# Kernel optimization log

Hardware: AMD Instinct MI355X
Metric: run time of the kernel (lower is better)

The kernel has to match this reference:

```python
import jax, jax.numpy as jnp
import numpy as np
from jax import lax

T, B, N_INP, N_HID, N_OUT = 512, 64, 64, 2048, 64


def setup_inputs() -> dict:
    key = jax.random.key(0)
    ks = jax.random.split(key, 8)
    scale = 0.9 / np.sqrt(N_HID)  # keep recurrence stable over T steps
    return {
        "x": jax.random.normal(ks[0], (T, B, N_INP), jnp.float32),
        "Wi_w": jax.random.normal(ks[1], (N_HID, N_INP), jnp.float32) / np.sqrt(N_INP),
        "Wi_b": jax.random.normal(ks[2], (N_HID,), jnp.float32) * 0.1,
        "Wh_w": jax.random.normal(ks[3], (N_HID, N_HID), jnp.float32) * scale,
        "A": jax.random.uniform(ks[4], (N_HID,), jnp.float32),
        "omega": jax.random.uniform(ks[5], (N_HID,), jnp.float32),
        "Wr_w": jax.random.normal(ks[6], (N_OUT, N_HID), jnp.float32) / np.sqrt(N_HID),
        "Wr_b": jax.random.normal(ks[7], (N_OUT,), jnp.float32) * 0.1,
    }


def reference(x, Wi_w, Wi_b, Wh_w, A, omega, Wr_w, Wr_b):
    # Precompute input projection for all timesteps: [T, B, n_hid]
    u = jnp.einsum("tbi,hi->tbh", x, Wi_w) + Wi_b
    state0 = jnp.ones((x.shape[1], Wh_w.shape[0]), x.dtype)

    def step(state, u_t):
        # state = A * cos(omega*state + Wi(x_t)) + Wh(state)
        new = A * jnp.cos(omega * state + u_t) + state @ Wh_w.T
        return new, None

    state, _ = lax.scan(step, state0, u)
    return state @ Wr_w.T + Wr_b  # readout on final state: [B, n_out]
```

## Files before the change

kernel.cpp:

```cpp
#include <hip/hip_runtime.h>


typedef _Float16 half_t;
typedef _Float16 half8 __attribute__((ext_vector_type(8)));
typedef float f32x4 __attribute__((ext_vector_type(4)));

#define NHID 2048
#define NOUT 64
#define ST_UNIT 65536
#define N_ROUNDS 256

#define MFMA16(A, B, C) __builtin_amdgcn_mfma_f32_16x16x32_f16(A, B, C, 0, 0, 0)


__device__ __forceinline__ half8 cvt8(float4 lo, float4 hi) {
  half8 h;
  h[0] = (half_t)lo.x; h[1] = (half_t)lo.y; h[2] = (half_t)lo.z; h[3] = (half_t)lo.w;
  h[4] = (half_t)hi.x; h[5] = (half_t)hi.y; h[6] = (half_t)hi.z; h[7] = (half_t)hi.w;
  return h;
}

__global__ void psrnn_init_kernel(unsigned* flags, uint4* st) {
  int g = blockIdx.x * blockDim.x + threadIdx.x;
  uint4 v; v.x = 0x3C003C00u; v.y = 0x3C003C00u; v.z = 0x3C003C00u; v.w = 0x3C003C00u;
  const int rep = g >> 12, local = g & 4095;
  st[rep * (ST_UNIT / 8) + local] = v;
  if (g < 1024) flags[g] = 0;
}

__global__ __launch_bounds__(256) void psrnn_transpose_kernel(
    const float* __restrict__ Wh, half_t* __restrict__ WT16) {
  __shared__ float tile[64][65];
  const int bi = blockIdx.x & 31, bj = blockIdx.x >> 5;
  const int rs = threadIdx.x >> 6, c = threadIdx.x & 63;
#pragma unroll
  for (int i = 0; i < 16; ++i) {
    const int row = rs * 16 + i;
    tile[row][c] = Wh[(size_t)(bi * 64 + row) * NHID + bj * 64 + c];
  }
  __syncthreads();
#pragma unroll
  for (int i = 0; i < 16; ++i) {
    const int row = rs * 16 + i;
    WT16[(size_t)(bj * 64 + row) * NHID + bi * 64 + c] = (half_t)tile[c][row];
  }
}

__global__ __launch_bounds__(256) void psrnn_w2_kernel(
    const float* __restrict__ Wh, const half_t* __restrict__ WT16,
    half_t* __restrict__ W2) {
  const int bi = blockIdx.x & 31, bj = blockIdx.x >> 5;
  const int w = threadIdx.x >> 6, lane = threadIdx.x & 63;
  const int lm = lane & 15, kg = lane >> 4;
  const int rowA = bi * 64 + w * 16 + lm;
  f32x4 acc[4];
#pragma unroll
  for (int bt = 0; bt < 4; ++bt) acc[bt] = (f32x4){0.f, 0.f, 0.f, 0.f};
  for (int c = 0; c < 64; ++c) {
    const float* pa = Wh + (size_t)rowA * NHID + c * 32 + kg * 8;
    half8 a = cvt8(*(const float4*)pa, *(const float4*)(pa + 4));
#pragma unroll
    for (int bt = 0; bt < 4; ++bt) {
      half8 b = *(const half8*)(WT16 + (size_t)(bj * 64 + bt * 16 + lm) * NHID + c * 32 + kg * 8);
      acc[bt] = MFMA16(a, b, acc[bt]);
    }
  }
#pragma unroll
  for (int bt = 0; bt < 4; ++bt)
#pragma unroll
    for (int r = 0; r < 4; ++r)
      W2[(size_t)(bi * 64 + w * 16 + kg * 4 + r) * NHID + bj * 64 + bt * 16 + lm] =
          (half_t)acc[bt][r];
}

__global__ __launch_bounds__(256, 1) void psrnn_main_kernel(
    const float* __restrict__ x,
    const float* __restrict__ Wi_w,
    const float* __restrict__ Wi_b,
    const float* __restrict__ Wh_w,
    const float* __restrict__ Av,
    const float* __restrict__ Om,
    const half_t* __restrict__ W2,
    unsigned* __restrict__ flags,
    half_t* __restrict__ St)
{
  __shared__ float ybuf[2][4][2][2][16][18];
  __shared__ float ubuf[2][2][2][16][18];

  const int tid = threadIdx.x, w = tid >> 6, lane = tid & 63;
  const int lm = lane & 15, kg = lane >> 4;
  const int rep = blockIdx.x & 3, slot = blockIdx.x >> 2;
  const int n0 = slot * 32, b0 = rep * 16;
  const int tpar = w >> 1, ntu = w & 1;

  half8 wb[2][16], w2b[2][16];
#pragma unroll
  for (int nt = 0; nt < 2; ++nt)
#pragma unroll
    for (int c = 0; c < 16; ++c) {
      const float* p = Wh_w + (size_t)(n0 + nt * 16 + lm) * NHID + (w * 512 + c * 32 + kg * 8);
      wb[nt][c] = cvt8(*(const float4*)p, *(const float4*)(p + 4));
      w2b[nt][c] = *(const half8*)(W2 + (size_t)(n0 + nt * 16 + lm) * NHID +
                                   (w * 512 + c * 32 + kg * 8));
    }
  half8 wi0, wi1;
  {
    const float* p = Wi_w + (size_t)(n0 + ntu * 16 + lm) * 64 + kg * 8;
    wi0 = cvt8(*(const float4*)p, *(const float4*)(p + 4));
    wi1 = cvt8(*(const float4*)(p + 32), *(const float4*)(p + 36));
  }

  const int m = tid >> 4, nn = tid & 15;
  float cA2[2], cOm2[2], cB2[2];
  int off2[2];
#pragma unroll
  for (int nt = 0; nt < 2; ++nt) {
    const int ng = n0 + nt * 16 + nn;
    cA2[nt] = Av[ng]; cOm2[nt] = Om[ng]; cB2[nt] = Wi_b[ng];
    off2[nt] = ((slot * 4 + nt * 2 + (nn >> 3)) * 16 + m) * 8 + (nn & 7);
  }
  float cpr[2];

  unsigned* const pollp = flags + rep * 256 + w * 64 + lane;
  unsigned* const myf   = flags + rep * 256 + slot * 4 + w;

  if (w < 2) {
    const float* xp = x + (size_t)(b0 + lm) * 64;
    float4 a0 = *(const float4*)(xp + kg * 8), a1 = *(const float4*)(xp + kg * 8 + 4);
    float4 a2 = *(const float4*)(xp + 32 + kg * 8), a3 = *(const float4*)(xp + 36 + kg * 8);
    f32x4 au = {0.f, 0.f, 0.f, 0.f};
    au = MFMA16(cvt8(a0, a1), wi0, au);
    au = MFMA16(cvt8(a2, a3), wi1, au);
#pragma unroll
    for (int r = 0; r < 4; ++r) ubuf[0][0][ntu][kg * 4 + r][lm] = au[r];
  }
  __syncthreads();
  {
    half_t* w0c = St + (size_t)rep * ST_UNIT + 32768;
#pragma unroll
    for (int nt = 0; nt < 2; ++nt) {
      const float u0 = ubuf[0][0][nt][m][nn] + cB2[nt];
      cpr[nt] = cA2[nt] * __cosf(cOm2[nt] * 1.0f + u0);
      unsigned hv = (unsigned)__builtin_bit_cast(unsigned short, (half_t)cpr[nt]);
      const half_t* sp = w0c + off2[nt];
      asm volatile("global_store_short %0, %1, off sc1" :: "v"(sp), "v"(hv) : "memory");
    }
    asm volatile("s_waitcnt vmcnt(0)" ::: "memory");
    if (lane == 0)
      __hip_atomic_store(myf, 1u, __ATOMIC_RELAXED, __HIP_MEMORY_SCOPE_AGENT);
  }
  float4 xr0, xr1, xr2, xr3;
  {
    const float* xp = x + ((size_t)(1 + tpar) * 64 + b0 + lm) * 64;
    xr0 = *(const float4*)(xp + kg * 8);  xr1 = *(const float4*)(xp + kg * 8 + 4);
    xr2 = *(const float4*)(xp + 32 + kg * 8); xr3 = *(const float4*)(xp + 36 + kg * 8);
  }

  int bR = 0;
  for (int k = 0; k < N_ROUNDS; ++k) {
    const int bW = (bR == 2) ? 0 : bR + 1;
    const half_t* rB = St + (size_t)(bR * 4 + rep) * ST_UNIT;
    half_t* wB       = St + (size_t)(bW * 4 + rep) * ST_UNIT;
    const int par = k & 1;

    {
      f32x4 au = {0.f, 0.f, 0.f, 0.f};
      au = MFMA16(cvt8(xr0, xr1), wi0, au);
      au = MFMA16(cvt8(xr2, xr3), wi1, au);
#pragma unroll
      for (int r = 0; r < 4; ++r) ubuf[par][tpar][ntu][kg * 4 + r][lm] = au[r];
    }

    {
      const unsigned tgt = (unsigned)(k + 1);
      unsigned v = __hip_atomic_load(pollp, __ATOMIC_RELAXED, __HIP_MEMORY_SCOPE_AGENT);
      while (!__all((int)(v >= tgt)))
        v = __hip_atomic_load(pollp, __ATOMIC_RELAXED, __HIP_MEMORY_SCOPE_AGENT);
    }

    const half_t* ps0 = rB + (w * 16) * 512 + kg * 128 + lm * 8;
    const half_t* ps1 = ps0 + 2048;
    const half_t* ps2 = ps0 + 4096;
    const half_t* ps3 = ps0 + 6144;
    const half_t* pc0 = ps0 + 32768;
    const half_t* pc1 = ps1 + 32768;
    const half_t* pc2 = ps2 + 32768;
    const half_t* pc3 = ps3 + 32768;
    float4 Sr[16], Cr[16];
    asm volatile(
        "global_load_dwordx4 %0, %32, off sc1\n\t"
        "global_load_dwordx4 %1, %32, off offset:1024 sc1\n\t"
        "global_load_dwordx4 %2, %32, off offset:2048 sc1\n\t"
        "global_load_dwordx4 %3, %32, off offset:3072 sc1\n\t"
        "global_load_dwordx4 %4, %33, off sc1\n\t"
        "global_load_dwordx4 %5, %33, off offset:1024 sc1\n\t"
        "global_load_dwordx4 %6, %33, off offset:2048 sc1\n\t"
        "global_load_dwordx4 %7, %33, off offset:3072 sc1\n\t"
        "global_load_dwordx4 %8, %34, off sc1\n\t"
        "global_load_dwordx4 %9, %34, off offset:1024 sc1\n\t"
        "global_load_dwordx4 %10, %34, off offset:2048 sc1\n\t"
        "global_load_dwordx4 %11, %34, off offset:3072 sc1\n\t"
        "global_load_dwordx4 %12, %35, off sc1\n\t"
        "global_load_dwordx4 %13, %35, off offset:1024 sc1\n\t"
        "global_load_dwordx4 %14, %35, off offset:2048 sc1\n\t"
        "global_load_dwordx4 %15, %35, off offset:3072 sc1\n\t"
        "global_load_dwordx4 %16, %36, off sc1\n\t"
        "global_load_dwordx4 %17, %36, off offset:1024 sc1\n\t"
        "global_load_dwordx4 %18, %36, off offset:2048 sc1\n\t"
        "global_load_dwordx4 %19, %36, off offset:3072 sc1\n\t"
        "global_load_dwordx4 %20, %37, off sc1\n\t"
        "global_load_dwordx4 %21, %37, off offset:1024 sc1\n\t"
        "global_load_dwordx4 %22, %37, off offset:2048 sc1\n\t"
        "global_load_dwordx4 %23, %37, off offset:3072 sc1\n\t"
        "global_load_dwordx4 %24, %38, off sc1\n\t"
        "global_load_dwordx4 %25, %38, off offset:1024 sc1\n\t"
        "global_load_dwordx4 %26, %38, off offset:2048 sc1\n\t"
        "global_load_dwordx4 %27, %38, off offset:3072 sc1\n\t"
        "global_load_dwordx4 %28, %39, off sc1\n\t"
        "global_load_dwordx4 %29, %39, off offset:1024 sc1\n\t"
        "global_load_dwordx4 %30, %39, off offset:2048 sc1\n\t"
        "global_load_dwordx4 %31, %39, off offset:3072 sc1\n\t"
        "s_waitcnt vmcnt(0)"
        : "=&v"(Sr[0]), "=&v"(Sr[1]), "=&v"(Sr[2]), "=&v"(Sr[3]),
          "=&v"(Sr[4]), "=&v"(Sr[5]), "=&v"(Sr[6]), "=&v"(Sr[7]),
          "=&v"(Sr[8]), "=&v"(Sr[9]), "=&v"(Sr[10]), "=&v"(Sr[11]),
          "=&v"(Sr[12]), "=&v"(Sr[13]), "=&v"(Sr[14]), "=&v"(Sr[15]),
          "=&v"(Cr[0]), "=&v"(Cr[1]), "=&v"(Cr[2]), "=&v"(Cr[3]),
          "=&v"(Cr[4]), "=&v"(Cr[5]), "=&v"(Cr[6]), "=&v"(Cr[7]),
          "=&v"(Cr[8]), "=&v"(Cr[9]), "=&v"(Cr[10]), "=&v"(Cr[11]),
          "=&v"(Cr[12]), "=&v"(Cr[13]), "=&v"(Cr[14]), "=&v"(Cr[15])
        : "v"(ps0), "v"(ps1), "v"(ps2), "v"(ps3),
          "v"(pc0), "v"(pc1), "v"(pc2), "v"(pc3)
        : "memory");

    f32x4 y1a0 = {0.f,0.f,0.f,0.f}, y1a1 = {0.f,0.f,0.f,0.f};
    f32x4 y23a0 = {0.f,0.f,0.f,0.f}, y23a1 = {0.f,0.f,0.f,0.f};
#pragma unroll
    for (int c = 0; c < 16; ++c) {
      half8 sf = __builtin_bit_cast(half8, Sr[c]);
      half8 cf = __builtin_bit_cast(half8, Cr[c]);
      y1a0 = MFMA16(sf, wb[0][c], y1a0);
      y1a1 = MFMA16(sf, wb[1][c], y1a1);
      y23a0 = MFMA16(cf, wb[0][c], y23a0);
      y23a1 = MFMA16(cf, wb[1][c], y23a1);
      y23a0 = MFMA16(sf, w2b[0][c], y23a0);
      y23a1 = MFMA16(sf, w2b[1][c], y23a1);
    }
#pragma unroll
    for (int r = 0; r < 4; ++r) {
      ybuf[par][w][0][0][kg * 4 + r][lm] = y1a0[r];
      ybuf[par][w][0][1][kg * 4 + r][lm] = y1a1[r];
      ybuf[par][w][1][0][kg * 4 + r][lm] = y23a0[r];
      ybuf[par][w][1][1][kg * 4 + r][lm] = y23a1[r];
    }
    __syncthreads();

#pragma unroll
    for (int nt = 0; nt < 2; ++nt) {
      const float y1v = ybuf[par][0][0][nt][m][nn] + ybuf[par][1][0][nt][m][nn] +
                        ybuf[par][2][0][nt][m][nn] + ybuf[par][3][0][nt][m][nn];
      const float y23v = ybuf[par][0][1][nt][m][nn] + ybuf[par][1][1][nt][m][nn] +
                         ybuf[par][2][1][nt][m][nn] + ybuf[par][3][1][nt][m][nn];
      const float u1 = ubuf[par][0][nt][m][nn] + cB2[nt];
      const float u2 = ubuf[par][1][nt][m][nn] + cB2[nt];
      const float s1 = cpr[nt] + y1v;
      const float c1 = cA2[nt] * __cosf(cOm2[nt] * s1 + u1);
      const float s2 = c1 + y23v;
      const float c2 = cA2[nt] * __cosf(cOm2[nt] * s2 + u2);
      cpr[nt] = c2;
      unsigned hs = (unsigned)__builtin_bit_cast(unsigned short, (half_t)s2);
      unsigned hc = (unsigned)__builtin_bit_cast(unsigned short, (half_t)c2);
      const half_t* sps = wB + off2[nt];
      const half_t* spc = wB + 32768 + off2[nt];
      asm volatile("global_store_short %0, %1, off sc1" :: "v"(sps), "v"(hs) : "memory");
      asm volatile("global_store_short %0, %1, off sc1" :: "v"(spc), "v"(hc) : "memory");
    }
    asm volatile("s_waitcnt vmcnt(0)" ::: "memory");
    if (lane == 0)
      __hip_atomic_store(myf, (unsigned)(k + 2), __ATOMIC_RELAXED, __HIP_MEMORY_SCOPE_AGENT);

    {
      int t = 2 * k + 3 + tpar;
      if (t > 511) t = 511;
      const float* xp = x + ((size_t)t * 64 + b0 + lm) * 64;
      xr0 = *(const float4*)(xp + kg * 8);  xr1 = *(const float4*)(xp + kg * 8 + 4);
      xr2 = *(const float4*)(xp + 32 + kg * 8); xr3 = *(const float4*)(xp + 36 + kg * 8);
    }
    bR = bW;
  }
}

__global__ __launch_bounds__(256) void psrnn_readout_kernel(
    const float* __restrict__ Wr_w,
    const float* __restrict__ Wr_b,
    const half_t* __restrict__ St,
    float* __restrict__ out)
{
  const int tid = threadIdx.x, v = tid >> 6, lane = tid & 63;
  const int lm = lane & 15, kg = lane >> 4;
  const int rep = blockIdx.x;
  const half_t* sb = St + (size_t)(1 * 4 + rep) * ST_UNIT;

  f32x4 acc = {0.f, 0.f, 0.f, 0.f};
  for (int cg = 0; cg < 64; ++cg) {
    half8 a = *(const half8*)(sb + (size_t)cg * 512 + kg * 128 + lm * 8);
    const float* p = Wr_w + (size_t)(v * 16 + lm) * NHID + cg * 32 + kg * 8;
    half8 b = cvt8(*(const float4*)p, *(const float4*)(p + 4));
    acc = MFMA16(a, b, acc);
  }
#pragma unroll
  for (int r = 0; r < 4; ++r) {
    const int bidx = rep * 16 + kg * 4 + r;
    out[bidx * NOUT + v * 16 + lm] = acc[r] + Wr_b[v * 16 + lm];
  }
}

extern "C" void kernel_launch(void* const* d_in, const int* in_sizes, int n_in,
                              void* d_out, int out_size, void* d_ws, size_t ws_size,
                              hipStream_t stream) {
  const float* x    = (const float*)d_in[0];
  const float* Wi_w = (const float*)d_in[1];
  const float* Wi_b = (const float*)d_in[2];
  const float* Wh_w = (const float*)d_in[3];
  const float* Av   = (const float*)d_in[4];
  const float* Om   = (const float*)d_in[5];
  const float* Wr_w = (const float*)d_in[6];
  const float* Wr_b = (const float*)d_in[7];

  unsigned* flags = (unsigned*)d_ws;
  half_t*   St    = (half_t*)((char*)d_ws + 4096);
  half_t*   W2    = (half_t*)((char*)d_ws + (2u << 20));
  half_t*   WT16  = (half_t*)((char*)d_ws + (2u << 20) + (8u << 20));

  psrnn_init_kernel<<<64, 256, 0, stream>>>(flags, (uint4*)St);
  psrnn_transpose_kernel<<<1024, 256, 0, stream>>>(Wh_w, WT16);
  psrnn_w2_kernel<<<1024, 256, 0, stream>>>(Wh_w, WT16, W2);
  psrnn_main_kernel<<<256, 256, 0, stream>>>(x, Wi_w, Wi_b, Wh_w, Av, Om, W2, flags, St);
  psrnn_readout_kernel<<<4, 256, 0, stream>>>(Wr_w, Wr_b, St, (float*)d_out);
}
```

Measured before the change: 1.280 ms.

## Map persistent blocks to XCDs and mirror state buffers for local-cache reads

The main recurrent kernel now reads the XCC id in hardware and assigns each block's batch replica and hidden slot from it through an atomic roster, so blocks of one replica share a die. The state is written twice: once with sc0 into a buffer read by local waves and once with sc1 into a buffer read by remote waves. This lets same-die readers hit a nearer cache level instead of going through the coherence point. The W2 precompute GEMM is also retiled to 128x128 blocks with an LDS-staged B operand, and dynamic LDS is requested to force one block per CU. The risks are that slot assignment depends on the hardware placing exactly 32 blocks on each XCD, and that the doubled stores add write traffic.

```diff
diff --git a/kernel.cpp b/kernel.cpp
--- a/kernel.cpp
+++ b/kernel.cpp
@@ -20,15 +20,18 @@
   return h;
 }
 
-__global__ void psrnn_init_kernel(unsigned* flags, uint4* st) {
+__global__ void psrnn_init_kernel(unsigned* flags, unsigned* roster,
+                                  uint4* stA, uint4* stB) {
   int g = blockIdx.x * blockDim.x + threadIdx.x;
   uint4 v; v.x = 0x3C003C00u; v.y = 0x3C003C00u; v.z = 0x3C003C00u; v.w = 0x3C003C00u;
   const int rep = g >> 12, local = g & 4095;
-  st[rep * (ST_UNIT / 8) + local] = v;
+  stA[rep * (ST_UNIT / 8) + local] = v;
+  stB[rep * (ST_UNIT / 8) + local] = v;
   if (g < 1024) flags[g] = 0;
-}
-
-__global__ __launch_bounds__(256) void psrnn_transpose_kernel(
+  else if (g < 1032) roster[g - 1024] = 0;
+}
+
+__global__ __launch_bounds__(256) void psrnn_conv_kernel(
     const float* __restrict__ Wh, half_t* __restrict__ WT16) {
   __shared__ float tile[64][65];
   const int bi = blockIdx.x & 31, bj = blockIdx.x >> 5;
@@ -49,28 +52,46 @@
 __global__ __launch_bounds__(256) void psrnn_w2_kernel(
     const float* __restrict__ Wh, const half_t* __restrict__ WT16,
     half_t* __restrict__ W2) {
-  const int bi = blockIdx.x & 31, bj = blockIdx.x >> 5;
-  const int w = threadIdx.x >> 6, lane = threadIdx.x & 63;
+  __shared__ half_t Bs[128][40];
+  const int bi = blockIdx.x & 15, bj = blockIdx.x >> 4;
+  const int tid = threadIdx.x, w = tid >> 6, lane = tid & 63;
   const int lm = lane & 15, kg = lane >> 4;
-  const int rowA = bi * 64 + w * 16 + lm;
-  f32x4 acc[4];
-#pragma unroll
-  for (int bt = 0; bt < 4; ++bt) acc[bt] = (f32x4){0.f, 0.f, 0.f, 0.f};
+  const int brow = tid >> 2, bseg = tid & 3;
+
+  f32x4 acc[2][8];
+#pragma unroll
+  for (int mt = 0; mt < 2; ++mt)
+#pragma unroll
+    for (int nt = 0; nt < 8; ++nt) acc[mt][nt] = (f32x4){0.f, 0.f, 0.f, 0.f};
+
   for (int c = 0; c < 64; ++c) {
-    const float* pa = Wh + (size_t)rowA * NHID + c * 32 + kg * 8;
-    half8 a = cvt8(*(const float4*)pa, *(const float4*)(pa + 4));
-#pragma unroll
-    for (int bt = 0; bt < 4; ++bt) {
-      half8 b = *(const half8*)(WT16 + (size_t)(bj * 64 + bt * 16 + lm) * NHID + c * 32 + kg * 8);
-      acc[bt] = MFMA16(a, b, acc[bt]);
-    }
-  }
-#pragma unroll
-  for (int bt = 0; bt < 4; ++bt)
-#pragma unroll
-    for (int r = 0; r < 4; ++r)
-      W2[(size_t)(bi * 64 + w * 16 + kg * 4 + r) * NHID + bj * 64 + bt * 16 + lm] =
-          (half_t)acc[bt][r];
+    __syncthreads();
+#pragma unroll
+    for (int i = 0; i < 2; ++i) {
+      const int row = brow + i * 64;
+      *(half8*)&Bs[row][bseg * 8] =
+          *(const half8*)(WT16 + (size_t)(bj * 128 + row) * NHID + c * 32 + bseg * 8);
+    }
+    __syncthreads();
+    const float* pa0 = Wh + (size_t)(bi * 128 + w * 32 + lm) * NHID + c * 32 + kg * 8;
+    const float* pa1 = pa0 + (size_t)16 * NHID;
+    half8 a0 = cvt8(*(const float4*)pa0, *(const float4*)(pa0 + 4));
+    half8 a1 = cvt8(*(const float4*)pa1, *(const float4*)(pa1 + 4));
+#pragma unroll
+    for (int nt = 0; nt < 8; ++nt) {
+      half8 b = *(const half8*)&Bs[nt * 16 + lm][kg * 8];
+      acc[0][nt] = MFMA16(a0, b, acc[0][nt]);
+      acc[1][nt] = MFMA16(a1, b, acc[1][nt]);
+    }
+  }
+#pragma unroll
+  for (int mt = 0; mt < 2; ++mt)
+#pragma unroll
+    for (int nt = 0; nt < 8; ++nt)
+#pragma unroll
+      for (int r = 0; r < 4; ++r)
+        W2[(size_t)(bi * 128 + w * 32 + mt * 16 + kg * 4 + r) * NHID +
+           bj * 128 + nt * 16 + lm] = (half_t)acc[mt][nt][r];
 }
 
 __global__ __launch_bounds__(256, 1) void psrnn_main_kernel(
@@ -82,15 +103,28 @@
     const float* __restrict__ Om,
     const half_t* __restrict__ W2,
     unsigned* __restrict__ flags,
-    half_t* __restrict__ St)
+    unsigned* __restrict__ roster,
+    half_t* __restrict__ StA,
+    half_t* __restrict__ StB)
 {
+  extern __shared__ char lds_force[];
   __shared__ float ybuf[2][4][2][2][16][18];
   __shared__ float ubuf[2][2][2][16][18];
+  __shared__ unsigned slot_sh;
+  (void)lds_force;
 
   const int tid = threadIdx.x, w = tid >> 6, lane = tid & 63;
   const int lm = lane & 15, kg = lane >> 4;
-  const int rep = blockIdx.x & 3, slot = blockIdx.x >> 2;
+
+  unsigned xcd;
+  asm volatile("s_getreg_b32 %0, hwreg(HW_REG_XCC_ID)" : "=s"(xcd));
+  const int rep    = (int)(xcd & 3u);
+  const int halfId = (int)((xcd >> 2) & 1u);
+  if (tid == 0) slot_sh = (unsigned)(halfId * 32) + (atomicAdd(&roster[xcd & 7u], 1u) & 31u);
+  __syncthreads();
+  const int slot = (int)slot_sh;
   const int n0 = slot * 32, b0 = rep * 16;
+  const bool locw = ((w >> 1) == halfId);
   const int tpar = w >> 1, ntu = w & 1;
 
   half8 wb[2][16], w2b[2][16];
@@ -136,14 +170,17 @@
   }
   __syncthreads();
   {
-    half_t* w0c = St + (size_t)rep * ST_UNIT + 32768;
+    half_t* cA_ = StA + (size_t)rep * ST_UNIT + 32768;
+    half_t* cB_ = StB + (size_t)rep * ST_UNIT + 32768;
 #pragma unroll
     for (int nt = 0; nt < 2; ++nt) {
       const float u0 = ubuf[0][0][nt][m][nn] + cB2[nt];
       cpr[nt] = cA2[nt] * __cosf(cOm2[nt] * 1.0f + u0);
       unsigned hv = (unsigned)__builtin_bit_cast(unsigned short, (half_t)cpr[nt]);
-      const half_t* sp = w0c + off2[nt];
-      asm volatile("global_store_short %0, %1, off sc1" :: "v"(sp), "v"(hv) : "memory");
+      const half_t* pA = cA_ + off2[nt];
+      const half_t* pB = cB_ + off2[nt];
+      asm volatile("global_store_short %0, %1, off sc0" :: "v"(pA), "v"(hv) : "memory");
+      asm volatile("global_store_short %0, %1, off sc1" :: "v"(pB), "v"(hv) : "memory");
     }
     asm volatile("s_waitcnt vmcnt(0)" ::: "memory");
     if (lane == 0)
@@ -159,8 +196,6 @@
   int bR = 0;
   for (int k = 0; k < N_ROUNDS; ++k) {
     const int bW = (bR == 2) ? 0 : bR + 1;
-    const half_t* rB = St + (size_t)(bR * 4 + rep) * ST_UNIT;
-    half_t* wB       = St + (size_t)(bW * 4 + rep) * ST_UNIT;
     const int par = k & 1;
 
     {
@@ -178,7 +213,8 @@
         v = __hip_atomic_load(pollp, __ATOMIC_RELAXED, __HIP_MEMORY_SCOPE_AGENT);
     }
 
-    const half_t* ps0 = rB + (w * 16) * 512 + kg * 128 + lm * 8;
+    const half_t* rb = (locw ? StA : StB) + (size_t)(bR * 4 + rep) * ST_UNIT;
+    const half_t* ps0 = rb + w * 8192 + kg * 128 + lm * 8;
     const half_t* ps1 = ps0 + 2048;
     const half_t* ps2 = ps0 + 4096;
     const half_t* ps3 = ps0 + 6144;
@@ -187,51 +223,54 @@
     const half_t* pc2 = ps2 + 32768;
     const half_t* pc3 = ps3 + 32768;
     float4 Sr[16], Cr[16];
-    asm volatile(
-        "global_load_dwordx4 %0, %32, off sc1\n\t"
-        "global_load_dwordx4 %1, %32, off offset:1024 sc1\n\t"
-        "global_load_dwordx4 %2, %32, off offset:2048 sc1\n\t"
-        "global_load_dwordx4 %3, %32, off offset:3072 sc1\n\t"
-        "global_load_dwordx4 %4, %33, off sc1\n\t"
-        "global_load_dwordx4 %5, %33, off offset:1024 sc1\n\t"
-        "global_load_dwordx4 %6, %33, off offset:2048 sc1\n\t"
-        "global_load_dwordx4 %7, %33, off offset:3072 sc1\n\t"
-        "global_load_dwordx4 %8, %34, off sc1\n\t"
-        "global_load_dwordx4 %9, %34, off offset:1024 sc1\n\t"
-        "global_load_dwordx4 %10, %34, off offset:2048 sc1\n\t"
-        "global_load_dwordx4 %11, %34, off offset:3072 sc1\n\t"
-        "global_load_dwordx4 %12, %35, off sc1\n\t"
-        "global_load_dwordx4 %13, %35, off offset:1024 sc1\n\t"
-        "global_load_dwordx4 %14, %35, off offset:2048 sc1\n\t"
-        "global_load_dwordx4 %15, %35, off offset:3072 sc1\n\t"
-        "global_load_dwordx4 %16, %36, off sc1\n\t"
-        "global_load_dwordx4 %17, %36, off offset:1024 sc1\n\t"
-        "global_load_dwordx4 %18, %36, off offset:2048 sc1\n\t"
-        "global_load_dwordx4 %19, %36, off offset:3072 sc1\n\t"
-        "global_load_dwordx4 %20, %37, off sc1\n\t"
-        "global_load_dwordx4 %21, %37, off offset:1024 sc1\n\t"
-        "global_load_dwordx4 %22, %37, off offset:2048 sc1\n\t"
-        "global_load_dwordx4 %23, %37, off offset:3072 sc1\n\t"
-        "global_load_dwordx4 %24, %38, off sc1\n\t"
-        "global_load_dwordx4 %25, %38, off offset:1024 sc1\n\t"
-        "global_load_dwordx4 %26, %38, off offset:2048 sc1\n\t"
-        "global_load_dwordx4 %27, %38, off offset:3072 sc1\n\t"
-        "global_load_dwordx4 %28, %39, off sc1\n\t"
-        "global_load_dwordx4 %29, %39, off offset:1024 sc1\n\t"
-        "global_load_dwordx4 %30, %39, off offset:2048 sc1\n\t"
-        "global_load_dwordx4 %31, %39, off offset:3072 sc1\n\t"
-        "s_waitcnt vmcnt(0)"
-        : "=&v"(Sr[0]), "=&v"(Sr[1]), "=&v"(Sr[2]), "=&v"(Sr[3]),
-          "=&v"(Sr[4]), "=&v"(Sr[5]), "=&v"(Sr[6]), "=&v"(Sr[7]),
-          "=&v"(Sr[8]), "=&v"(Sr[9]), "=&v"(Sr[10]), "=&v"(Sr[11]),
-          "=&v"(Sr[12]), "=&v"(Sr[13]), "=&v"(Sr[14]), "=&v"(Sr[15]),
-          "=&v"(Cr[0]), "=&v"(Cr[1]), "=&v"(Cr[2]), "=&v"(Cr[3]),
-          "=&v"(Cr[4]), "=&v"(Cr[5]), "=&v"(Cr[6]), "=&v"(Cr[7]),
-          "=&v"(Cr[8]), "=&v"(Cr[9]), "=&v"(Cr[10]), "=&v"(Cr[11]),
-          "=&v"(Cr[12]), "=&v"(Cr[13]), "=&v"(Cr[14]), "=&v"(Cr[15])
-        : "v"(ps0), "v"(ps1), "v"(ps2), "v"(ps3),
-          "v"(pc0), "v"(pc1), "v"(pc2), "v"(pc3)
-        : "memory");
+#define LOADS(SC)                                                         \
+    asm volatile(                                                         \
+        "global_load_dwordx4 %0, %32, off " SC "\n\t"                     \
+        "global_load_dwordx4 %1, %32, off offset:1024 " SC "\n\t"         \
+        "global_load_dwordx4 %2, %32, off offset:2048 " SC "\n\t"         \
+        "global_load_dwordx4 %3, %32, off offset:3072 " SC "\n\t"         \
+        "global_load_dwordx4 %4, %33, off " SC "\n\t"                     \
+        "global_load_dwordx4 %5, %33, off offset:1024 " SC "\n\t"         \
+        "global_load_dwordx4 %6, %33, off offset:2048 " SC "\n\t"         \
+        "global_load_dwordx4 %7, %33, off offset:3072 " SC "\n\t"         \
+        "global_load_dwordx4 %8, %34, off " SC "\n\t"                     \
+        "global_load_dwordx4 %9, %34, off offset:1024 " SC "\n\t"         \
+        "global_load_dwordx4 %10, %34, off offset:2048 " SC "\n\t"        \
+        "global_load_dwordx4 %11, %34, off offset:3072 " SC "\n\t"        \
+        "global_load_dwordx4 %12, %35, off " SC "\n\t"                    \
+        "global_load_dwordx4 %13, %35, off offset:1024 " SC "\n\t"        \
+        "global_load_dwordx4 %14, %35, off offset:2048 " SC "\n\t"        \
+        "global_load_dwordx4 %15, %35, off offset:3072 " SC "\n\t"        \
+        "global_load_dwordx4 %16, %36, off " SC "\n\t"                    \
+        "global_load_dwordx4 %17, %36, off offset:1024 " SC "\n\t"        \
+        "global_load_dwordx4 %18, %36, off offset:2048 " SC "\n\t"        \
+        "global_load_dwordx4 %19, %36, off offset:3072 " SC "\n\t"        \
+        "global_load_dwordx4 %20, %37, off " SC "\n\t"                    \
+        "global_load_dwordx4 %21, %37, off offset:1024 " SC "\n\t"        \
+        "global_load_dwordx4 %22, %37, off offset:2048 " SC "\n\t"        \
+        "global_load_dwordx4 %23, %37, off offset:3072 " SC "\n\t"        \
+        "global_load_dwordx4 %24, %38, off " SC "\n\t"                    \
+        "global_load_dwordx4 %25, %38, off offset:1024 " SC "\n\t"        \
+        "global_load_dwordx4 %26, %38, off offset:2048 " SC "\n\t"        \
+        "global_load_dwordx4 %27, %38, off offset:3072 " SC "\n\t"        \
+        "global_load_dwordx4 %28, %39, off " SC "\n\t"                    \
+        "global_load_dwordx4 %29, %39, off offset:1024 " SC "\n\t"        \
+        "global_load_dwordx4 %30, %39, off offset:2048 " SC "\n\t"        \
+        "global_load_dwordx4 %31, %39, off offset:3072 " SC "\n\t"        \
+        "s_waitcnt vmcnt(0)"                                              \
+        : "=&v"(Sr[0]), "=&v"(Sr[1]), "=&v"(Sr[2]), "=&v"(Sr[3]),         \
+          "=&v"(Sr[4]), "=&v"(Sr[5]), "=&v"(Sr[6]), "=&v"(Sr[7]),         \
+          "=&v"(Sr[8]), "=&v"(Sr[9]), "=&v"(Sr[10]), "=&v"(Sr[11]),       \
+          "=&v"(Sr[12]), "=&v"(Sr[13]), "=&v"(Sr[14]), "=&v"(Sr[15]),     \
+          "=&v"(Cr[0]), "=&v"(Cr[1]), "=&v"(Cr[2]), "=&v"(Cr[3]),         \
+          "=&v"(Cr[4]), "=&v"(Cr[5]), "=&v"(Cr[6]), "=&v"(Cr[7]),         \
+          "=&v"(Cr[8]), "=&v"(Cr[9]), "=&v"(Cr[10]), "=&v"(Cr[11]),       \
+          "=&v"(Cr[12]), "=&v"(Cr[13]), "=&v"(Cr[14]), "=&v"(Cr[15])      \
+        : "v"(ps0), "v"(ps1), "v"(ps2), "v"(ps3),                         \
+          "v"(pc0), "v"(pc1), "v"(pc2), "v"(pc3)                          \
+        : "memory")
+    if (locw) { LOADS("sc0"); } else { LOADS("sc1"); }
+#undef LOADS
 
     f32x4 y1a0 = {0.f,0.f,0.f,0.f}, y1a1 = {0.f,0.f,0.f,0.f};
     f32x4 y23a0 = {0.f,0.f,0.f,0.f}, y23a1 = {0.f,0.f,0.f,0.f};
@@ -255,6 +294,8 @@
     }
     __syncthreads();
 
+    half_t* wBA = StA + (size_t)(bW * 4 + rep) * ST_UNIT;
+    half_t* wBB = StB + (size_t)(bW * 4 + rep) * ST_UNIT;
 #pragma unroll
     for (int nt = 0; nt < 2; ++nt) {
       const float y1v = ybuf[par][0][0][nt][m][nn] + ybuf[par][1][0][nt][m][nn] +
@@ -270,10 +311,14 @@
       cpr[nt] = c2;
       unsigned hs = (unsigned)__builtin_bit_cast(unsigned short, (half_t)s2);
       unsigned hc = (unsigned)__builtin_bit_cast(unsigned short, (half_t)c2);
-      const half_t* sps = wB + off2[nt];
-      const half_t* spc = wB + 32768 + off2[nt];
-      asm volatile("global_store_short %0, %1, off sc1" :: "v"(sps), "v"(hs) : "memory");
-      asm volatile("global_store_short %0, %1, off sc1" :: "v"(spc), "v"(hc) : "memory");
+      const half_t* sA = wBA + off2[nt];
+      const half_t* sB = wBB + off2[nt];
+      const half_t* cAp = wBA + 32768 + off2[nt];
+      const half_t* cBp = wBB + 32768 + off2[nt];
+      asm volatile("global_store_short %0, %1, off sc0" :: "v"(sA), "v"(hs) : "memory");
+      asm volatile("global_store_short %0, %1, off sc1" :: "v"(sB), "v"(hs) : "memory");
+      asm volatile("global_store_short %0, %1, off sc0" :: "v"(cAp), "v"(hc) : "memory");
+      asm volatile("global_store_short %0, %1, off sc1" :: "v"(cBp), "v"(hc) : "memory");
     }
     asm volatile("s_waitcnt vmcnt(0)" ::: "memory");
     if (lane == 0)
@@ -293,13 +338,13 @@
 __global__ __launch_bounds__(256) void psrnn_readout_kernel(
     const float* __restrict__ Wr_w,
     const float* __restrict__ Wr_b,
-    const half_t* __restrict__ St,
+    const half_t* __restrict__ StB,
     float* __restrict__ out)
 {
   const int tid = threadIdx.x, v = tid >> 6, lane = tid & 63;
   const int lm = lane & 15, kg = lane >> 4;
   const int rep = blockIdx.x;
-  const half_t* sb = St + (size_t)(1 * 4 + rep) * ST_UNIT;
+  const half_t* sb = StB + (size_t)(1 * 4 + rep) * ST_UNIT;
 
   f32x4 acc = {0.f, 0.f, 0.f, 0.f};
   for (int cg = 0; cg < 64; ++cg) {
@@ -327,14 +372,17 @@
   const float* Wr_w = (const float*)d_in[6];
   const float* Wr_b = (const float*)d_in[7];
 
-  unsigned* flags = (unsigned*)d_ws;
-  half_t*   St    = (half_t*)((char*)d_ws + 4096);
-  half_t*   W2    = (half_t*)((char*)d_ws + (2u << 20));
-  half_t*   WT16  = (half_t*)((char*)d_ws + (2u << 20) + (8u << 20));
-
-  psrnn_init_kernel<<<64, 256, 0, stream>>>(flags, (uint4*)St);
-  psrnn_transpose_kernel<<<1024, 256, 0, stream>>>(Wh_w, WT16);
-  psrnn_w2_kernel<<<1024, 256, 0, stream>>>(Wh_w, WT16, W2);
-  psrnn_main_kernel<<<256, 256, 0, stream>>>(x, Wi_w, Wi_b, Wh_w, Av, Om, W2, flags, St);
-  psrnn_readout_kernel<<<4, 256, 0, stream>>>(Wr_w, Wr_b, St, (float*)d_out);
-}
+  unsigned* flags  = (unsigned*)d_ws;
+  unsigned* roster = (unsigned*)((char*)d_ws + 4096);
+  half_t*   StA    = (half_t*)((char*)d_ws + (1u << 20));
+  half_t*   StB    = (half_t*)((char*)d_ws + (3u << 20));
+  half_t*   WT16   = (half_t*)((char*)d_ws + (8u << 20));
+  half_t*   W2     = (half_t*)((char*)d_ws + (16u << 20));
+
+  psrnn_conv_kernel<<<1024, 256, 0, stream>>>(Wh_w, WT16);
+  psrnn_w2_kernel<<<256, 256, 0, stream>>>(Wh_w, WT16, W2);
+  psrnn_init_kernel<<<64, 256, 0, stream>>>(flags, roster, (uint4*)StA, (uint4*)StB);
+  psrnn_main_kernel<<<256, 256, 40960, stream>>>(x, Wi_w, Wi_b, Wh_w, Av, Om, W2,
+                                                 flags, roster, StA, StB);
+  psrnn_readout_kernel<<<4, 256, 0, stream>>>(Wr_w, Wr_b, StB, (float*)d_out);
+}
```

After: 1.211 ms. -5.4%, faster.

## Interleave state/cos layout and retile W2 precompute GEMM through LDS

Applied to the files above, without the earlier changes.

Changes the global state buffer layout so the s and cos halves are interleaved per 16-byte group. Each thread now writes one packed dword pair per step instead of four scattered shorts. The K ordering of the weight fragments is permuted to match, using interleaving converts. The W2 = Wh·Wh GEMM is retiled to 128x128 blocks with the B tile staged in shared memory, reducing redundant global loads. The risk is in the permutation bookkeeping: k-index orderings must stay consistent across the main, readout and init kernels.

```diff
diff --git a/kernel.cpp b/kernel.cpp
--- a/kernel.cpp
+++ b/kernel.cpp
@@ -2,6 +2,7 @@
 
 
 typedef _Float16 half_t;
+typedef _Float16 half4 __attribute__((ext_vector_type(4)));
 typedef _Float16 half8 __attribute__((ext_vector_type(8)));
 typedef float f32x4 __attribute__((ext_vector_type(4)));
 
@@ -19,16 +20,32 @@
   h[4] = (half_t)hi.x; h[5] = (half_t)hi.y; h[6] = (half_t)hi.z; h[7] = (half_t)hi.w;
   return h;
 }
+__device__ __forceinline__ half8 cvt8i(float4 lo, float4 hi) {
+  half8 h;
+  h[0] = (half_t)lo.x; h[1] = (half_t)hi.x; h[2] = (half_t)lo.y; h[3] = (half_t)hi.y;
+  h[4] = (half_t)lo.z; h[5] = (half_t)hi.z; h[6] = (half_t)lo.w; h[7] = (half_t)hi.w;
+  return h;
+}
+__device__ __forceinline__ half8 ilv4(half4 lo, half4 hi) {
+  half8 h;
+  h[0] = lo[0]; h[1] = hi[0]; h[2] = lo[1]; h[3] = hi[1];
+  h[4] = lo[2]; h[5] = hi[2]; h[6] = lo[3]; h[7] = hi[3];
+  return h;
+}
 
 __global__ void psrnn_init_kernel(unsigned* flags, uint4* st) {
   int g = blockIdx.x * blockDim.x + threadIdx.x;
-  uint4 v; v.x = 0x3C003C00u; v.y = 0x3C003C00u; v.z = 0x3C003C00u; v.w = 0x3C003C00u;
-  const int rep = g >> 12, local = g & 4095;
-  st[rep * (ST_UNIT / 8) + local] = v;
+  uint4 one; one.x = 0x3C003C00u; one.y = 0x3C003C00u; one.z = 0x3C003C00u; one.w = 0x3C003C00u;
+  uint4 zer; zer.x = 0; zer.y = 0; zer.z = 0; zer.w = 0;
+#pragma unroll
+  for (int rr = 0; rr < 2; ++rr) {
+    const int gg = g + rr * 16384;
+    st[gg] = (gg & 1) ? zer : one;
+  }
   if (g < 1024) flags[g] = 0;
 }
 
-__global__ __launch_bounds__(256) void psrnn_transpose_kernel(
+__global__ __launch_bounds__(256) void psrnn_conv_kernel(
     const float* __restrict__ Wh, half_t* __restrict__ WT16) {
   __shared__ float tile[64][65];
   const int bi = blockIdx.x & 31, bj = blockIdx.x >> 5;
@@ -49,28 +66,46 @@
 __global__ __launch_bounds__(256) void psrnn_w2_kernel(
     const float* __restrict__ Wh, const half_t* __restrict__ WT16,
     half_t* __restrict__ W2) {
-  const int bi = blockIdx.x & 31, bj = blockIdx.x >> 5;
-  const int w = threadIdx.x >> 6, lane = threadIdx.x & 63;
+  __shared__ half_t Bs[128][40];
+  const int bi = blockIdx.x & 15, bj = blockIdx.x >> 4;
+  const int tid = threadIdx.x, w = tid >> 6, lane = tid & 63;
   const int lm = lane & 15, kg = lane >> 4;
-  const int rowA = bi * 64 + w * 16 + lm;
-  f32x4 acc[4];
-#pragma unroll
-  for (int bt = 0; bt < 4; ++bt) acc[bt] = (f32x4){0.f, 0.f, 0.f, 0.f};
+  const int brow = tid >> 2, bseg = tid & 3;
+
+  f32x4 acc[2][8];
+#pragma unroll
+  for (int mt = 0; mt < 2; ++mt)
+#pragma unroll
+    for (int nt = 0; nt < 8; ++nt) acc[mt][nt] = (f32x4){0.f, 0.f, 0.f, 0.f};
+
   for (int c = 0; c < 64; ++c) {
-    const float* pa = Wh + (size_t)rowA * NHID + c * 32 + kg * 8;
-    half8 a = cvt8(*(const float4*)pa, *(const float4*)(pa + 4));
-#pragma unroll
-    for (int bt = 0; bt < 4; ++bt) {
-      half8 b = *(const half8*)(WT16 + (size_t)(bj * 64 + bt * 16 + lm) * NHID + c * 32 + kg * 8);
-      acc[bt] = MFMA16(a, b, acc[bt]);
-    }
-  }
-#pragma unroll
-  for (int bt = 0; bt < 4; ++bt)
-#pragma unroll
-    for (int r = 0; r < 4; ++r)
-      W2[(size_t)(bi * 64 + w * 16 + kg * 4 + r) * NHID + bj * 64 + bt * 16 + lm] =
-          (half_t)acc[bt][r];
+    __syncthreads();
+#pragma unroll
+    for (int i = 0; i < 2; ++i) {
+      const int row = brow + i * 64;
+      *(half8*)&Bs[row][bseg * 8] =
+          *(const half8*)(WT16 + (size_t)(bj * 128 + row) * NHID + c * 32 + bseg * 8);
+    }
+    __syncthreads();
+    const float* pa0 = Wh + (size_t)(bi * 128 + w * 32 + lm) * NHID + c * 32 + kg * 8;
+    const float* pa1 = pa0 + (size_t)16 * NHID;
+    half8 a0 = cvt8(*(const float4*)pa0, *(const float4*)(pa0 + 4));
+    half8 a1 = cvt8(*(const float4*)pa1, *(const float4*)(pa1 + 4));
+#pragma unroll
+    for (int nt = 0; nt < 8; ++nt) {
+      half8 b = *(const half8*)&Bs[nt * 16 + lm][kg * 8];
+      acc[0][nt] = MFMA16(a0, b, acc[0][nt]);
+      acc[1][nt] = MFMA16(a1, b, acc[1][nt]);
+    }
+  }
+#pragma unroll
+  for (int mt = 0; mt < 2; ++mt)
+#pragma unroll
+    for (int nt = 0; nt < 8; ++nt)
+#pragma unroll
+      for (int r = 0; r < 4; ++r)
+        W2[(size_t)(bi * 128 + w * 32 + mt * 16 + kg * 4 + r) * NHID +
+           bj * 128 + nt * 16 + lm] = (half_t)acc[mt][nt][r];
 }
 
 __global__ __launch_bounds__(256, 1) void psrnn_main_kernel(
@@ -98,10 +133,11 @@
   for (int nt = 0; nt < 2; ++nt)
 #pragma unroll
     for (int c = 0; c < 16; ++c) {
-      const float* p = Wh_w + (size_t)(n0 + nt * 16 + lm) * NHID + (w * 512 + c * 32 + kg * 8);
-      wb[nt][c] = cvt8(*(const float4*)p, *(const float4*)(p + 4));
-      w2b[nt][c] = *(const half8*)(W2 + (size_t)(n0 + nt * 16 + lm) * NHID +
-                                   (w * 512 + c * 32 + kg * 8));
+      const size_t row = (size_t)(n0 + nt * 16 + lm);
+      const float* p = Wh_w + row * NHID + (w * 512 + c * 32 + kg * 4);
+      wb[nt][c] = cvt8i(*(const float4*)p, *(const float4*)(p + 16));
+      const half_t* q = W2 + row * NHID + (w * 512 + c * 32 + kg * 4);
+      w2b[nt][c] = ilv4(*(const half4*)q, *(const half4*)(q + 16));
     }
   half8 wi0, wi1;
   {
@@ -112,13 +148,12 @@
 
   const int m = tid >> 4, nn = tid & 15;
   float cA2[2], cOm2[2], cB2[2];
-  int off2[2];
 #pragma unroll
   for (int nt = 0; nt < 2; ++nt) {
     const int ng = n0 + nt * 16 + nn;
     cA2[nt] = Av[ng]; cOm2[nt] = Om[ng]; cB2[nt] = Wi_b[ng];
-    off2[nt] = ((slot * 4 + nt * 2 + (nn >> 3)) * 16 + m) * 8 + (nn & 7);
-  }
+  }
+  const int offp = (slot * 4 + (nn >> 2)) * 256 + m * 16 + (nn & 3) * 2;
   float cpr[2];
 
   unsigned* const pollp = flags + rep * 256 + w * 64 + lane;
@@ -136,15 +171,15 @@
   }
   __syncthreads();
   {
-    half_t* w0c = St + (size_t)rep * ST_UNIT + 32768;
 #pragma unroll
     for (int nt = 0; nt < 2; ++nt) {
       const float u0 = ubuf[0][0][nt][m][nn] + cB2[nt];
       cpr[nt] = cA2[nt] * __cosf(cOm2[nt] * 1.0f + u0);
-      unsigned hv = (unsigned)__builtin_bit_cast(unsigned short, (half_t)cpr[nt]);
-      const half_t* sp = w0c + off2[nt];
-      asm volatile("global_store_short %0, %1, off sc1" :: "v"(sp), "v"(hv) : "memory");
-    }
+    }
+    unsigned dc = (unsigned)__builtin_bit_cast(unsigned short, (half_t)cpr[0]) |
+                  ((unsigned)__builtin_bit_cast(unsigned short, (half_t)cpr[1]) << 16);
+    const half_t* cp = St + (size_t)rep * ST_UNIT + offp + 8;
+    asm volatile("global_store_dword %0, %1, off sc1" :: "v"(cp), "v"(dc) : "memory");
     asm volatile("s_waitcnt vmcnt(0)" ::: "memory");
     if (lane == 0)
       __hip_atomic_store(myf, 1u, __ATOMIC_RELAXED, __HIP_MEMORY_SCOPE_AGENT);
@@ -178,48 +213,48 @@
         v = __hip_atomic_load(pollp, __ATOMIC_RELAXED, __HIP_MEMORY_SCOPE_AGENT);
     }
 
-    const half_t* ps0 = rB + (w * 16) * 512 + kg * 128 + lm * 8;
-    const half_t* ps1 = ps0 + 2048;
-    const half_t* ps2 = ps0 + 4096;
-    const half_t* ps3 = ps0 + 6144;
-    const half_t* pc0 = ps0 + 32768;
-    const half_t* pc1 = ps1 + 32768;
-    const half_t* pc2 = ps2 + 32768;
-    const half_t* pc3 = ps3 + 32768;
+    const half_t* pb0 = rB + (size_t)(64 * w + 0  + kg) * 256 + lm * 16;
+    const half_t* pb1 = rB + (size_t)(64 * w + 8  + kg) * 256 + lm * 16;
+    const half_t* pb2 = rB + (size_t)(64 * w + 16 + kg) * 256 + lm * 16;
+    const half_t* pb3 = rB + (size_t)(64 * w + 24 + kg) * 256 + lm * 16;
+    const half_t* pb4 = rB + (size_t)(64 * w + 32 + kg) * 256 + lm * 16;
+    const half_t* pb5 = rB + (size_t)(64 * w + 40 + kg) * 256 + lm * 16;
+    const half_t* pb6 = rB + (size_t)(64 * w + 48 + kg) * 256 + lm * 16;
+    const half_t* pb7 = rB + (size_t)(64 * w + 56 + kg) * 256 + lm * 16;
     float4 Sr[16], Cr[16];
     asm volatile(
         "global_load_dwordx4 %0, %32, off sc1\n\t"
-        "global_load_dwordx4 %1, %32, off offset:1024 sc1\n\t"
-        "global_load_dwordx4 %2, %32, off offset:2048 sc1\n\t"
-        "global_load_dwordx4 %3, %32, off offset:3072 sc1\n\t"
-        "global_load_dwordx4 %4, %33, off sc1\n\t"
-        "global_load_dwordx4 %5, %33, off offset:1024 sc1\n\t"
-        "global_load_dwordx4 %6, %33, off offset:2048 sc1\n\t"
-        "global_load_dwordx4 %7, %33, off offset:3072 sc1\n\t"
-        "global_load_dwordx4 %8, %34, off sc1\n\t"
-        "global_load_dwordx4 %9, %34, off offset:1024 sc1\n\t"
-        "global_load_dwordx4 %10, %34, off offset:2048 sc1\n\t"
-        "global_load_dwordx4 %11, %34, off offset:3072 sc1\n\t"
-        "global_load_dwordx4 %12, %35, off sc1\n\t"
-        "global_load_dwordx4 %13, %35, off offset:1024 sc1\n\t"
-        "global_load_dwordx4 %14, %35, off offset:2048 sc1\n\t"
-        "global_load_dwordx4 %15, %35, off offset:3072 sc1\n\t"
-        "global_load_dwordx4 %16, %36, off sc1\n\t"
-        "global_load_dwordx4 %17, %36, off offset:1024 sc1\n\t"
-        "global_load_dwordx4 %18, %36, off offset:2048 sc1\n\t"
-        "global_load_dwordx4 %19, %36, off offset:3072 sc1\n\t"
-        "global_load_dwordx4 %20, %37, off sc1\n\t"
-        "global_load_dwordx4 %21, %37, off offset:1024 sc1\n\t"
-        "global_load_dwordx4 %22, %37, off offset:2048 sc1\n\t"
-        "global_load_dwordx4 %23, %37, off offset:3072 sc1\n\t"
-        "global_load_dwordx4 %24, %38, off sc1\n\t"
-        "global_load_dwordx4 %25, %38, off offset:1024 sc1\n\t"
-        "global_load_dwordx4 %26, %38, off offset:2048 sc1\n\t"
-        "global_load_dwordx4 %27, %38, off offset:3072 sc1\n\t"
-        "global_load_dwordx4 %28, %39, off sc1\n\t"
-        "global_load_dwordx4 %29, %39, off offset:1024 sc1\n\t"
-        "global_load_dwordx4 %30, %39, off offset:2048 sc1\n\t"
-        "global_load_dwordx4 %31, %39, off offset:3072 sc1\n\t"
+        "global_load_dwordx4 %1, %32, off offset:2048 sc1\n\t"
+        "global_load_dwordx4 %16, %32, off offset:16 sc1\n\t"
+        "global_load_dwordx4 %17, %32, off offset:2064 sc1\n\t"
+        "global_load_dwordx4 %2, %33, off sc1\n\t"
+        "global_load_dwordx4 %3, %33, off offset:2048 sc1\n\t"
+        "global_load_dwordx4 %18, %33, off offset:16 sc1\n\t"
+        "global_load_dwordx4 %19, %33, off offset:2064 sc1\n\t"
+        "global_load_dwordx4 %4, %34, off sc1\n\t"
+        "global_load_dwordx4 %5, %34, off offset:2048 sc1\n\t"
+        "global_load_dwordx4 %20, %34, off offset:16 sc1\n\t"
+        "global_load_dwordx4 %21, %34, off offset:2064 sc1\n\t"
+        "global_load_dwordx4 %6, %35, off sc1\n\t"
+        "global_load_dwordx4 %7, %35, off offset:2048 sc1\n\t"
+        "global_load_dwordx4 %22, %35, off offset:16 sc1\n\t"
+        "global_load_dwordx4 %23, %35, off offset:2064 sc1\n\t"
+        "global_load_dwordx4 %8, %36, off sc1\n\t"
+        "global_load_dwordx4 %9, %36, off offset:2048 sc1\n\t"
+        "global_load_dwordx4 %24, %36, off offset:16 sc1\n\t"
+        "global_load_dwordx4 %25, %36, off offset:2064 sc1\n\t"
+        "global_load_dwordx4 %10, %37, off sc1\n\t"
+        "global_load_dwordx4 %11, %37, off offset:2048 sc1\n\t"
+        "global_load_dwordx4 %26, %37, off offset:16 sc1\n\t"
+        "global_load_dwordx4 %27, %37, off offset:2064 sc1\n\t"
+        "global_load_dwordx4 %12, %38, off sc1\n\t"
+        "global_load_dwordx4 %13, %38, off offset:2048 sc1\n\t"
+        "global_load_dwordx4 %28, %38, off offset:16 sc1\n\t"
+        "global_load_dwordx4 %29, %38, off offset:2064 sc1\n\t"
+        "global_load_dwordx4 %14, %39, off sc1\n\t"
+        "global_load_dwordx4 %15, %39, off offset:2048 sc1\n\t"
+        "global_load_dwordx4 %30, %39, off offset:16 sc1\n\t"
+        "global_load_dwordx4 %31, %39, off offset:2064 sc1\n\t"
         "s_waitcnt vmcnt(0)"
         : "=&v"(Sr[0]), "=&v"(Sr[1]), "=&v"(Sr[2]), "=&v"(Sr[3]),
           "=&v"(Sr[4]), "=&v"(Sr[5]), "=&v"(Sr[6]), "=&v"(Sr[7]),
@@ -229,8 +264,8 @@
           "=&v"(Cr[4]), "=&v"(Cr[5]), "=&v"(Cr[6]), "=&v"(Cr[7]),
           "=&v"(Cr[8]), "=&v"(Cr[9]), "=&v"(Cr[10]), "=&v"(Cr[11]),
           "=&v"(Cr[12]), "=&v"(Cr[13]), "=&v"(Cr[14]), "=&v"(Cr[15])
-        : "v"(ps0), "v"(ps1), "v"(ps2), "v"(ps3),
-          "v"(pc0), "v"(pc1), "v"(pc2), "v"(pc3)
+        : "v"(pb0), "v"(pb1), "v"(pb2), "v"(pb3),
+          "v"(pb4), "v"(pb5), "v"(pb6), "v"(pb7)
         : "memory");
 
     f32x4 y1a0 = {0.f,0.f,0.f,0.f}, y1a1 = {0.f,0.f,0.f,0.f};
@@ -255,6 +290,7 @@
     }
     __syncthreads();
 
+    float s2v[2], c2v[2];
 #pragma unroll
     for (int nt = 0; nt < 2; ++nt) {
       const float y1v = ybuf[par][0][0][nt][m][nn] + ybuf[par][1][0][nt][m][nn] +
@@ -267,13 +303,18 @@
       const float c1 = cA2[nt] * __cosf(cOm2[nt] * s1 + u1);
       const float s2 = c1 + y23v;
       const float c2 = cA2[nt] * __cosf(cOm2[nt] * s2 + u2);
-      cpr[nt] = c2;
-      unsigned hs = (unsigned)__builtin_bit_cast(unsigned short, (half_t)s2);
-      unsigned hc = (unsigned)__builtin_bit_cast(unsigned short, (half_t)c2);
-      const half_t* sps = wB + off2[nt];
-      const half_t* spc = wB + 32768 + off2[nt];
-      asm volatile("global_store_short %0, %1, off sc1" :: "v"(sps), "v"(hs) : "memory");
-      asm volatile("global_store_short %0, %1, off sc1" :: "v"(spc), "v"(hc) : "memory");
+      cpr[nt] = c2; s2v[nt] = s2; c2v[nt] = c2;
+    }
+    {
+      unsigned ds = (unsigned)__builtin_bit_cast(unsigned short, (half_t)s2v[0]) |
+                    ((unsigned)__builtin_bit_cast(unsigned short, (half_t)s2v[1]) << 16);
+      unsigned dc = (unsigned)__builtin_bit_cast(unsigned short, (half_t)c2v[0]) |
+                    ((unsigned)__builtin_bit_cast(unsigned short, (half_t)c2v[1]) << 16);
+      const half_t* sp = wB + offp;
+      asm volatile(
+          "global_store_dword %0, %1, off sc1\n\t"
+          "global_store_dword %0, %2, off offset:16 sc1"
+          :: "v"(sp), "v"(ds), "v"(dc) : "memory");
     }
     asm volatile("s_waitcnt vmcnt(0)" ::: "memory");
     if (lane == 0)
@@ -303,9 +344,9 @@
 
   f32x4 acc = {0.f, 0.f, 0.f, 0.f};
   for (int cg = 0; cg < 64; ++cg) {
-    half8 a = *(const half8*)(sb + (size_t)cg * 512 + kg * 128 + lm * 8);
-    const float* p = Wr_w + (size_t)(v * 16 + lm) * NHID + cg * 32 + kg * 8;
-    half8 b = cvt8(*(const float4*)p, *(const float4*)(p + 4));
+    half8 a = *(const half8*)(sb + (size_t)(cg * 4 + kg) * 256 + lm * 16);
+    const float* p = Wr_w + (size_t)(v * 16 + lm) * NHID + cg * 32 + kg * 4;
+    half8 b = cvt8i(*(const float4*)p, *(const float4*)(p + 16));
     acc = MFMA16(a, b, acc);
   }
 #pragma unroll
@@ -328,13 +369,13 @@
   const float* Wr_b = (const float*)d_in[7];
 
   unsigned* flags = (unsigned*)d_ws;
-  half_t*   St    = (half_t*)((char*)d_ws + 4096);
-  half_t*   W2    = (half_t*)((char*)d_ws + (2u << 20));
-  half_t*   WT16  = (half_t*)((char*)d_ws + (2u << 20) + (8u << 20));
-
+  half_t*   St    = (half_t*)((char*)d_ws + (1u << 20));
+  half_t*   WT16  = (half_t*)((char*)d_ws + (8u << 20));
+  half_t*   W2    = (half_t*)((char*)d_ws + (16u << 20));
+
+  psrnn_conv_kernel<<<1024, 256, 0, stream>>>(Wh_w, WT16);
+  psrnn_w2_kernel<<<256, 256, 0, stream>>>(Wh_w, WT16, W2);
   psrnn_init_kernel<<<64, 256, 0, stream>>>(flags, (uint4*)St);
-  psrnn_transpose_kernel<<<1024, 256, 0, stream>>>(Wh_w, WT16);
-  psrnn_w2_kernel<<<1024, 256, 0, stream>>>(Wh_w, WT16, W2);
   psrnn_main_kernel<<<256, 256, 0, stream>>>(x, Wi_w, Wi_b, Wh_w, Av, Om, W2, flags, St);
   psrnn_readout_kernel<<<4, 256, 0, stream>>>(Wr_w, Wr_b, St, (float*)d_out);
 }
```

Measured after the change: 1.430 ms. 11.7% more time.
